# Kernel tuning notes

Hardware: AMD Instinct MI355X
Metric: run time of the kernel (lower is better)

The kernel has to match this reference:

```python
import jax, jax.numpy as jnp
import numpy as np

S = 512          # number of scenes (sequences)
P = 128          # pedestrians per scene
G = 16           # groups per scene (labels 1..G, each of size P//G)
D_IN, D_HID, D_OUT, D_FINAL = 256, 512, 16, 64


def setup_inputs() -> dict:
    key = jax.random.key(0)
    ks = jax.random.split(key, 10)
    B = S * P
    h_states = jax.random.normal(ks[0], (B, D_IN), dtype=jnp.float32)
    end_pos = jax.random.normal(ks[1], (B, 2), dtype=jnp.float32)
    starts = jnp.arange(S, dtype=jnp.int64) * P
    seq_start_end = jnp.stack([starts, starts + P], axis=1)
    # labels 1..G within each scene; every group present -> n_group = G (static)
    end_group = ((jnp.arange(B, dtype=jnp.int64) % G) + 1).reshape(B, 1)
    s = 0.05  # scale randn params to keep activations tame
    W_intra_0 = s * jax.random.normal(ks[2], (D_IN, D_HID), dtype=jnp.float32)
    W_intra_1 = s * jax.random.normal(ks[3], (D_HID, D_OUT), dtype=jnp.float32)
    W_inter_0 = s * jax.random.normal(ks[4], (D_OUT, D_HID), dtype=jnp.float32)
    W_inter_1 = s * jax.random.normal(ks[5], (D_HID, D_OUT), dtype=jnp.float32)
    out_W = s * jax.random.normal(ks[6], (2 * D_OUT, D_FINAL), dtype=jnp.float32)
    out_b = jnp.zeros((D_FINAL,), dtype=jnp.float32)
    return {"h_states": h_states, "end_pos": end_pos,
            "seq_start_end": seq_start_end, "end_group": end_group,
            "W_intra_0": W_intra_0, "W_intra_1": W_intra_1,
            "W_inter_0": W_inter_0, "W_inter_1": W_inter_1,
            "out_W": out_W, "out_b": out_b}


def reference(h_states, end_pos, seq_start_end, end_group,
              W_intra_0, W_intra_1, W_inter_0, W_inter_1, out_W, out_b):
    B = h_states.shape[0]
    num_seq = seq_start_end.shape[0]
    P_ = B // num_seq
    labels = end_group.reshape(num_seq, P_)
    h_seq = h_states.reshape(num_seq, P_, -1)
    eye = jnp.eye(P_, dtype=bool)
    grp_ids = jnp.arange(1, G + 1)

    def per_scene(h, lab):
        # intra-group adjacency: same nonzero group, plus self loops
        M = ((lab[:, None] == lab[None, :]) & (lab[:, None] != 0)) | eye
        Mf = M.astype(h.dtype)
        A = Mf / jnp.sum(Mf, axis=1, keepdims=True)          # row-normalize
        H = jax.nn.relu((A @ h) @ W_intra_0)
        H_intra = jax.nn.relu((A @ H) @ W_intra_1)           # (P, D_OUT)
        # GPool: unique rows of M == one-hot group membership (all labels nonzero)
        onehot = (lab[None, :] == grp_ids[:, None]).astype(h.dtype)  # (G, P)
        R = onehot / jnp.sum(onehot, axis=1, keepdims=True)
        Hg = R @ H_intra                                     # (G, D_OUT)
        # inter-group GCN over fully-connected normalized adjacency
        Ai = jnp.full((G, G), 1.0 / G, dtype=h.dtype)
        Hg = jax.nn.relu((Ai @ Hg) @ W_inter_0)
        Hg = jax.nn.relu((Ai @ Hg) @ W_inter_1)
        H_inter = R.T @ Hg                                   # GUnpool: (P, D_OUT)
        cat = jnp.concatenate([H_intra, H_inter], axis=1)    # (P, 2*D_OUT)
        return cat @ out_W + out_b

    out = jax.vmap(per_scene)(h_seq, labels)
    return out.reshape(B, -1)
```

## Files before the change

### kernel.cpp

```cpp
#include <hip/hip_runtime.h>
#include <hip/hip_bf16.h>

#define S_SCENES 512
#define P_PED    128
#define G_GRP    16
#define D_IN     256
#define D_HID    512
#define D_OUT    16
#define D_FINAL  64

typedef __bf16 bf16x8 __attribute__((ext_vector_type(8)));
typedef float  f32x4  __attribute__((ext_vector_type(4)));

#define HGS 264
#define Y1S 520

__device__ __forceinline__ unsigned short f2bf(float f) {
  unsigned int x; __builtin_memcpy(&x, &f, 4);
  unsigned int r = x + 0x7FFFu + ((x >> 16) & 1u);
  return (unsigned short)(r >> 16);
}

__global__ void build_wfrag(const float* __restrict__ W0,
                            const float* __restrict__ W1,
                            unsigned short* __restrict__ W0F,
                            unsigned short* __restrict__ W1F) {
  int e = blockIdx.x * blockDim.x + threadIdx.x;
  if (e < 131072) {
    int kb = e >> 9;
    int l  = (e >> 3) & 63;
    int j  = e & 7;
    int k8 = kb >> 5, nt = kb & 31;
    int k = k8 * 32 + ((l >> 4) << 3) + j;
    int n = nt * 16 + (l & 15);
    W0F[e] = f2bf(W0[k * 512 + n]);
  } else {
    int e2 = e - 131072;
    if (e2 < 8192) {
      int ks = e2 >> 9;
      int l  = (e2 >> 3) & 63;
      int j  = e2 & 7;
      int k = ks * 32 + ((l >> 4) << 3) + j;
      W1F[e2] = f2bf(W1[k * 16 + (l & 15)]);
    }
  }
}

__global__ __launch_bounds__(512) void scene_kernel(
    const float* __restrict__ h,
    const int* __restrict__ sse,
    const int* __restrict__ grp,
    const unsigned short* __restrict__ W0F,
    const unsigned short* __restrict__ W1F,
    const float* __restrict__ Wi0,
    const float* __restrict__ Wi1,
    const float* __restrict__ Wout,
    const float* __restrict__ bout,
    float* __restrict__ out)
{
  __shared__ int lab[P_PED];
  __shared__ int cnt[G_GRP];
  __shared__ int members[G_GRP][P_PED];
  __shared__ unsigned short hg[G_GRP * HGS];
  __shared__ unsigned short y1[G_GRP * Y1S];
  __shared__ float hg2p[8][G_GRP][D_OUT];
  __shared__ float hg2[G_GRP][D_OUT];
  __shared__ float mvec[D_OUT];
  __shared__ float t1v[D_HID];
  __shared__ float hiv[D_OUT];
  __shared__ float cvec[D_FINAL];
  __shared__ float orow[G_GRP * D_FINAL];

  const int t = threadIdx.x;
  const int s = blockIdx.x;
  const int is64 = (grp[1] == 0) ? 1 : 0;
  const int start = is64 ? sse[4 * s] : sse[2 * s];
  const int w = t >> 6;
  const int l = t & 63;
  const int m16 = l & 15;
  const int q = l >> 4;

  if (t < G_GRP) cnt[t] = 0;
  __syncthreads();
  if (t < P_PED) {
    int idx = start + t;
    int g = (is64 ? grp[2 * idx] : grp[idx]) - 1;
    if (g < 0) g = 0; if (g > G_GRP - 1) g = G_GRP - 1;
    lab[t] = g;
    int slot = atomicAdd(&cnt[g], 1);
    if (slot < P_PED) members[g][slot] = t;
  }
  __syncthreads();

  for (int it = 0; it < 2; ++it) {
    int item = t + it * 512;
    int g  = item >> 6;
    int ch = item & 63;
    int cn = cnt[g];
    float a0 = 0.f, a1 = 0.f, a2 = 0.f, a3 = 0.f;
    const float* base = h + (size_t)start * D_IN + ch * 4;
    for (int m = 0; m < cn; ++m) {
      int p = members[g][m];
      float4 v = *(const float4*)(base + p * D_IN);
      a0 += v.x; a1 += v.y; a2 += v.z; a3 += v.w;
    }
    float inv = 1.0f / (float)(cn > 0 ? cn : 1);
    ushort4 o;
    o.x = f2bf(a0 * inv); o.y = f2bf(a1 * inv);
    o.z = f2bf(a2 * inv); o.w = f2bf(a3 * inv);
    *(ushort4*)&hg[g * HGS + ch * 4] = o;
  }
  __syncthreads();

  bf16x8 afr[8];
  #pragma unroll
  for (int k8 = 0; k8 < 8; ++k8)
    afr[k8] = *(const bf16x8*)&hg[m16 * HGS + k8 * 32 + q * 8];

  #pragma unroll
  for (int ntl = 0; ntl < 4; ++ntl) {
    int nt = w * 4 + ntl;
    f32x4 acc = {0.f, 0.f, 0.f, 0.f};
    #pragma unroll
    for (int k8 = 0; k8 < 8; ++k8) {
      bf16x8 bfr = *(const bf16x8*)(W0F + (size_t)(((k8 * 32 + nt) * 64) + l) * 8);
      acc = __builtin_amdgcn_mfma_f32_16x16x32_bf16(afr[k8], bfr, acc, 0, 0, 0);
    }
    #pragma unroll
    for (int r = 0; r < 4; ++r) {
      float v = acc[r];
      v = v > 0.f ? v : 0.f;
      y1[(q * 4 + r) * Y1S + nt * 16 + m16] = f2bf(v);
    }
  }
  __syncthreads();

  {
    f32x4 acc = {0.f, 0.f, 0.f, 0.f};
    #pragma unroll
    for (int kk = 0; kk < 2; ++kk) {
      int ks = w * 2 + kk;
      bf16x8 a2 = *(const bf16x8*)&y1[m16 * Y1S + ks * 32 + q * 8];
      bf16x8 b2 = *(const bf16x8*)(W1F + (size_t)(ks * 64 + l) * 8);
      acc = __builtin_amdgcn_mfma_f32_16x16x32_bf16(a2, b2, acc, 0, 0, 0);
    }
    #pragma unroll
    for (int r = 0; r < 4; ++r) hg2p[w][q * 4 + r][m16] = acc[r];
  }
  __syncthreads();
  if (t < 256) {
    int g = t >> 4, n = t & 15;
    float sum = 0.f;
    #pragma unroll
    for (int ww = 0; ww < 8; ++ww) sum += hg2p[ww][g][n];
    hg2[g][n] = sum > 0.f ? sum : 0.f;
  }
  __syncthreads();

  if (t < D_OUT) {
    float sm = 0.f;
    #pragma unroll
    for (int g = 0; g < G_GRP; ++g) sm += hg2[g][t];
    mvec[t] = sm * (1.0f / 16.0f);
  }
  __syncthreads();
  {
    float sm = 0.f;
    #pragma unroll
    for (int n = 0; n < D_OUT; ++n) sm += mvec[n] * Wi0[n * D_HID + t];
    t1v[t] = sm > 0.f ? sm : 0.f;
  }
  __syncthreads();
  #pragma unroll
  for (int nn = 0; nn < 2; ++nn) {
    int n = w * 2 + nn;
    float part = 0.f;
    #pragma unroll
    for (int r = 0; r < 8; ++r) {
      int j = l + r * 64;
      part += t1v[j] * Wi1[j * D_OUT + n];
    }
    for (int off = 32; off; off >>= 1) part += __shfl_down(part, off);
    if (l == 0) hiv[n] = part > 0.f ? part : 0.f;
  }
  __syncthreads();
  if (t < D_FINAL) {
    float sm = 0.f;
    #pragma unroll
    for (int n = 0; n < D_OUT; ++n)
      sm += hiv[n] * Wout[(G_GRP + n) * D_FINAL + t];
    cvec[t] = sm;
  }
  __syncthreads();

  for (int it = 0; it < 2; ++it) {
    int item = t + it * 512;
    int g = item >> 6, c = item & 63;
    float sm = 0.f;
    #pragma unroll
    for (int n = 0; n < D_OUT; ++n)
      sm += hg2[g][n] * Wout[n * D_FINAL + c];
    int cn = cnt[g];
    float inv = 1.0f / (float)(cn > 0 ? cn : 1);
    sm += cvec[c] * inv + bout[c];
    orow[g * D_FINAL + c] = sm;
  }
  __syncthreads();

  for (int it = 0; it < 4; ++it) {
    int i4 = t + it * 512;
    int p  = i4 >> 4;
    int c4 = i4 & 15;
    int g  = lab[p];
    float4 v = *(const float4*)&orow[g * D_FINAL + c4 * 4];
    *(float4*)(out + (size_t)(start + p) * D_FINAL + c4 * 4) = v;
  }
}

extern "C" void kernel_launch(void* const* d_in, const int* in_sizes, int n_in,
                              void* d_out, int out_size, void* d_ws, size_t ws_size,
                              hipStream_t stream) {
  const float* h    = (const float*)d_in[0];
  const int*   sse  = (const int*)d_in[2];
  const int*   grp  = (const int*)d_in[3];
  const float* W0   = (const float*)d_in[4];
  const float* W1   = (const float*)d_in[5];
  const float* Wi0  = (const float*)d_in[6];
  const float* Wi1  = (const float*)d_in[7];
  const float* Wout = (const float*)d_in[8];
  const float* bout = (const float*)d_in[9];

  unsigned short* W0F = (unsigned short*)d_ws;
  unsigned short* W1F = (unsigned short*)d_ws + 131072;

  build_wfrag<<<544, 256, 0, stream>>>(W0, W1, W0F, W1F);
  scene_kernel<<<S_SCENES, 512, 0, stream>>>(h, sse, grp, W0F, W1F,
                                             Wi0, Wi1, Wout, bout,
                                             (float*)d_out);
}
```

Measured before the change: 129.8 us.

## Unroll group gather loads, coalesce weight prep, shrink members and raise occupancy

The group-mean gather now handles two groups per thread at once. It has a fast path for groups of exactly 8, where the loop is fully unrolled so many independent global loads can be in flight. The weight fragment builder now reads W0/W1 in coalesced order and scatters the writes. The members array is stored as bytes to save LDS, and launch bounds request 2 blocks per CU to raise occupancy, which may force register spills.

```diff
diff --git a/kernel.cpp b/kernel.cpp
--- a/kernel.cpp
+++ b/kernel.cpp
@@ -25,28 +25,29 @@
                             const float* __restrict__ W1,
                             unsigned short* __restrict__ W0F,
                             unsigned short* __restrict__ W1F) {
-  int e = blockIdx.x * blockDim.x + threadIdx.x;
-  if (e < 131072) {
-    int kb = e >> 9;
-    int l  = (e >> 3) & 63;
-    int j  = e & 7;
-    int k8 = kb >> 5, nt = kb & 31;
-    int k = k8 * 32 + ((l >> 4) << 3) + j;
-    int n = nt * 16 + (l & 15);
-    W0F[e] = f2bf(W0[k * 512 + n]);
+  int tid = blockIdx.x * blockDim.x + threadIdx.x;
+  if (tid < 131072) {
+    int k = tid >> 9, n = tid & 511;
+    float v = W0[tid];
+    int k8 = k >> 5, kr = k & 31;
+    int j = kr & 7, lhi = kr >> 3;
+    int nt = n >> 4, n16 = n & 15;
+    int l = lhi * 16 + n16;
+    W0F[(((k8 * 32 + nt) * 64) + l) * 8 + j] = f2bf(v);
   } else {
-    int e2 = e - 131072;
-    if (e2 < 8192) {
-      int ks = e2 >> 9;
-      int l  = (e2 >> 3) & 63;
-      int j  = e2 & 7;
-      int k = ks * 32 + ((l >> 4) << 3) + j;
-      W1F[e2] = f2bf(W1[k * 16 + (l & 15)]);
-    }
-  }
-}
-
-__global__ __launch_bounds__(512) void scene_kernel(
+    int t2 = tid - 131072;
+    if (t2 < 8192) {
+      int k = t2 >> 4, n = t2 & 15;
+      float v = W1[t2];
+      int ks = k >> 5, kr = k & 31;
+      int j = kr & 7, lhi = kr >> 3;
+      int l = lhi * 16 + n;
+      W1F[((ks * 64) + l) * 8 + j] = f2bf(v);
+    }
+  }
+}
+
+__global__ __launch_bounds__(512, 2) void scene_kernel(
     const float* __restrict__ h,
     const int* __restrict__ sse,
     const int* __restrict__ grp,
@@ -60,7 +61,7 @@
 {
   __shared__ int lab[P_PED];
   __shared__ int cnt[G_GRP];
-  __shared__ int members[G_GRP][P_PED];
+  __shared__ unsigned char members[G_GRP][P_PED];
   __shared__ unsigned short hg[G_GRP * HGS];
   __shared__ unsigned short y1[G_GRP * Y1S];
   __shared__ float hg2p[8][G_GRP][D_OUT];
@@ -88,27 +89,37 @@
     if (g < 0) g = 0; if (g > G_GRP - 1) g = G_GRP - 1;
     lab[t] = g;
     int slot = atomicAdd(&cnt[g], 1);
-    if (slot < P_PED) members[g][slot] = t;
-  }
-  __syncthreads();
-
-  for (int it = 0; it < 2; ++it) {
-    int item = t + it * 512;
-    int g  = item >> 6;
-    int ch = item & 63;
-    int cn = cnt[g];
-    float a0 = 0.f, a1 = 0.f, a2 = 0.f, a3 = 0.f;
-    const float* base = h + (size_t)start * D_IN + ch * 4;
-    for (int m = 0; m < cn; ++m) {
-      int p = members[g][m];
-      float4 v = *(const float4*)(base + p * D_IN);
-      a0 += v.x; a1 += v.y; a2 += v.z; a3 += v.w;
-    }
-    float inv = 1.0f / (float)(cn > 0 ? cn : 1);
-    ushort4 o;
-    o.x = f2bf(a0 * inv); o.y = f2bf(a1 * inv);
-    o.z = f2bf(a2 * inv); o.w = f2bf(a3 * inv);
-    *(ushort4*)&hg[g * HGS + ch * 4] = o;
+    if (slot < P_PED) members[g][slot] = (unsigned char)t;
+  }
+  __syncthreads();
+
+  {
+    int g0 = w;
+    int g1 = w + 8;
+    int ch = (t & 63) << 2;
+    int cn0 = cnt[g0], cn1 = cnt[g1];
+    const float* base = h + (size_t)start * D_IN + ch;
+    f32x4 a0 = {0.f, 0.f, 0.f, 0.f}, a1 = {0.f, 0.f, 0.f, 0.f};
+    if (cn0 == 8 && cn1 == 8) {
+      #pragma unroll
+      for (int m = 0; m < 8; ++m) {
+        int p0 = members[g0][m];
+        int p1 = members[g1][m];
+        a0 += *(const f32x4*)(base + p0 * D_IN);
+        a1 += *(const f32x4*)(base + p1 * D_IN);
+      }
+      a0 *= 0.125f; a1 *= 0.125f;
+    } else {
+      for (int m = 0; m < cn0; ++m) a0 += *(const f32x4*)(base + members[g0][m] * D_IN);
+      for (int m = 0; m < cn1; ++m) a1 += *(const f32x4*)(base + members[g1][m] * D_IN);
+      a0 *= 1.0f / (float)(cn0 > 0 ? cn0 : 1);
+      a1 *= 1.0f / (float)(cn1 > 0 ? cn1 : 1);
+    }
+    ushort4 o0, o1;
+    o0.x = f2bf(a0[0]); o0.y = f2bf(a0[1]); o0.z = f2bf(a0[2]); o0.w = f2bf(a0[3]);
+    o1.x = f2bf(a1[0]); o1.y = f2bf(a1[1]); o1.z = f2bf(a1[2]); o1.w = f2bf(a1[3]);
+    *(ushort4*)&hg[g0 * HGS + ch] = o0;
+    *(ushort4*)&hg[g1 * HGS + ch] = o1;
   }
   __syncthreads();
 
```

Result: no change. 130.2 us (+0.2%).
